# Kernel optimization log

Hardware: AMD Instinct MI355X
Metric: run time of the kernel (lower is better)

## Reference

```python
import jax, jax.numpy as jnp
import numpy as np

B = 65536
OBS_DIM = 85          # input_shape
FEAT = 8              # dim_entity_feature
NL = 5                # dim_landmarks
NT = 10               # dim_total
INF = 64              # in_features == out_features
HID = 64              # rnn_hidden_dim
NACT = 5              # n_actions
ALPHA = 0.01


def _leaky(x):
    return jnp.where(x > 0, x, ALPHA * x)


def setup_inputs() -> dict:
    key = jax.random.key(0)
    ks = jax.random.split(key, 26)
    s = 0.1
    d = {
        'obs': jax.random.normal(ks[0], (B, OBS_DIM), jnp.float32),
        'hidden_state': jax.random.normal(ks[1], (B, HID), jnp.float32),
        # entity input projections (input_layer_0/1/2), stored [in, out]
        'w_in0': jax.random.normal(ks[2], (FEAT, INF), jnp.float32) * s,
        'b_in0': jax.random.normal(ks[3], (INF,), jnp.float32) * s,
        'w_in1': jax.random.normal(ks[4], (FEAT, INF), jnp.float32) * s,
        'b_in1': jax.random.normal(ks[5], (INF,), jnp.float32) * s,
        'w_in2': jax.random.normal(ks[6], (FEAT, INF), jnp.float32) * s,
        'b_in2': jax.random.normal(ks[7], (INF,), jnp.float32) * s,
        # GAT params
        'W': jax.random.normal(ks[8], (INF, INF), jnp.float32) * s,
        'a': jax.random.normal(ks[9], (2 * INF, 1), jnp.float32) * s,
        # output MLP on attention rows (dim_soft = 2*dim_nearby = 10)
        'w_o1': jax.random.normal(ks[10], (2 * NL, 32), jnp.float32) * s,
        'b_o1': jax.random.normal(ks[11], (32,), jnp.float32) * s,
        'w_o2': jax.random.normal(ks[12], (32, 16), jnp.float32) * s,
        'b_o2': jax.random.normal(ks[13], (16,), jnp.float32) * s,
        'w_o3': jax.random.normal(ks[14], (16, 1), jnp.float32) * s,
        'b_o3': jax.random.normal(ks[15], (1,), jnp.float32) * s,
        # fc1 takes obs (85) concat atom_plug (5) -> 90
        'w_fc1': jax.random.normal(ks[16], (OBS_DIM + NL, HID), jnp.float32) * s,
        'b_fc1': jax.random.normal(ks[17], (HID,), jnp.float32) * s,
        # GRUCell, torch layout: [3H, in]
        'w_ih': jax.random.normal(ks[18], (3 * HID, HID), jnp.float32) * s,
        'w_hh': jax.random.normal(ks[19], (3 * HID, HID), jnp.float32) * s,
        'b_ih': jax.random.normal(ks[20], (3 * HID,), jnp.float32) * s,
        'b_hh': jax.random.normal(ks[21], (3 * HID,), jnp.float32) * s,
        'w_fc2': jax.random.normal(ks[22], (HID, NACT), jnp.float32) * s,
        'b_fc2': jax.random.normal(ks[23], (NACT,), jnp.float32) * s,
    }
    return d


def reference(obs, hidden_state, w_in0, b_in0, w_in1, b_in1, w_in2, b_in2,
              W, a, w_o1, b_o1, w_o2, b_o2, w_o3, b_o3,
              w_fc1, b_fc1, w_ih, w_hh, b_ih, b_hh, w_fc2, b_fc2):
    # data_preprocess: drop last dim_nearby cols, rotate first 4 to back, reshape to entities
    o = obs[:, :OBS_DIM - NL]                               # [B, 80]
    obs_in = jnp.concatenate([o[:, 4:], o[:, :4]], axis=-1).reshape(-1, NT, FEAT)  # [B,10,8]

    h0 = _leaky(obs_in @ w_in0 + b_in0)                     # [B,10,64]
    h1 = _leaky(obs_in @ w_in1 + b_in1)
    h2 = _leaky(obs_in @ w_in2 + b_in2)
    h_mix = jnp.concatenate([h0[:, :NL], h1[:, NL:NT - 1], h2[:, NT - 1:NT]], axis=1)  # [B,10,64]

    Wh = h_mix @ W                                          # [B,10,64]
    Wh1 = Wh @ a[:INF]                                      # [B,10,1]
    Wh2 = Wh @ a[INF:]                                      # [B,10,1]
    e = _leaky(Wh1 + jnp.swapaxes(Wh2, 1, 2))               # [B,10,10]

    att0 = jax.nn.softmax(e[:, :NL, NL:], axis=-1)          # [B,5,5]
    att1 = jnp.swapaxes(jax.nn.softmax(e[:, NL:, :NL], axis=-1), 1, 2)  # [B,5,5]
    attention = jnp.concatenate([att0, att1], axis=-1)      # [B,5,10]

    hp = _leaky(attention @ w_o1 + b_o1)
    hp = _leaky(hp @ w_o2 + b_o2)
    hp = _leaky(hp @ w_o3 + b_o3)[..., 0]                   # [B,5]
    obs_out = jax.nn.softmax(hp, axis=-1)                   # [B,5]

    obs_comb = jnp.concatenate([obs, obs_out], axis=-1)     # [B,90]
    x = jax.nn.relu(obs_comb @ w_fc1 + b_fc1)               # [B,64]

    h_in = hidden_state.reshape(-1, HID)
    gi = x @ w_ih.T + b_ih                                  # [B,192]
    gh = h_in @ w_hh.T + b_hh
    r = jax.nn.sigmoid(gi[:, :HID] + gh[:, :HID])
    z = jax.nn.sigmoid(gi[:, HID:2 * HID] + gh[:, HID:2 * HID])
    n = jnp.tanh(gi[:, 2 * HID:] + r * gh[:, 2 * HID:])
    h = (1.0 - z) * n + z * h_in                            # [B,64]

    q = h @ w_fc2 + b_fc2                                   # [B,5]
    return (q, h)
```

## Files before the change

kernel.cpp:

```cpp
#include <hip/hip_runtime.h>
#include <math.h>

namespace {

typedef __bf16 bf16x8 __attribute__((ext_vector_type(8)));
typedef float  f32x4  __attribute__((ext_vector_type(4)));
typedef float  f32x2  __attribute__((ext_vector_type(2)));

constexpr int B_      = 65536;
constexpr int OBS_DIM_= 85;
constexpr int NL_     = 5;
constexpr int NT_     = 10;
constexpr int HID_    = 64;
constexpr int NACT_   = 5;
constexpr float ALPHA_= 0.01f;

__device__ __forceinline__ float leaky(float x)    { return fmaf(fminf(x, 0.0f), ALPHA_ - 1.0f, x); }
__device__ __forceinline__ float sigmoidf(float x) { return 1.0f / (1.0f + __expf(-x)); }
__device__ __forceinline__ float tanh_fast(float x){ return 1.0f - 2.0f / (__expf(2.0f * x) + 1.0f); }

__global__ void prep_kernel(const float* __restrict__ W, const float* __restrict__ a,
                            const float* __restrict__ w_ih, const float* __restrict__ w_hh,
                            const float* __restrict__ w_fc1, void* __restrict__ ws) {
  float* Wa   = (float*)ws;
  __bf16* ih  = (__bf16*)((char*)ws + 512);
  __bf16* hh  = ih + 192 * 64;
  __bf16* f1t = hh + 192 * 64;
  const int tid = blockIdx.x * 256 + threadIdx.x;
  if (blockIdx.x == 0 && threadIdx.x < 64) {
    const int i = threadIdx.x;
    float s1 = 0.0f, s2 = 0.0f;
    #pragma unroll
    for (int j = 0; j < 64; ++j) {
      float w = W[i * 64 + j];
      s1 += w * a[j];
      s2 += w * a[64 + j];
    }
    Wa[i] = s1;
    Wa[64 + i] = s2;
  }
  const int stride = gridDim.x * 256;
  for (int i = tid; i < 192 * 64; i += stride) {
    ih[i] = (__bf16)w_ih[i];
    hh[i] = (__bf16)w_hh[i];
  }
  for (int i = tid; i < 64 * 96; i += stride) {
    int n = i / 96, k = i - 96 * n;
    f1t[i] = (__bf16)(k < 90 ? w_fc1[k * 64 + n] : 0.0f);
  }
}


__global__ __launch_bounds__(256) void front_kernel(
    const float* __restrict__ obs,
    const float* __restrict__ w_in0, const float* __restrict__ b_in0,
    const float* __restrict__ w_in1, const float* __restrict__ b_in1,
    const float* __restrict__ w_in2, const float* __restrict__ b_in2,
    const float* __restrict__ w_o1, const float* __restrict__ b_o1,
    const float* __restrict__ w_o2, const float* __restrict__ b_o2,
    const float* __restrict__ w_o3, const float* __restrict__ b_o3,
    const float* __restrict__ Wa,
    float* __restrict__ out5) {

  __shared__ __align__(16) float s_obs[16][84];
  __shared__ float s_wh1[16][12], s_wh2[16][12];
  __shared__ float s_colm[16][6], s_cols[16][6];
  __shared__ __align__(16) float s_att[16][5][12];
  __shared__ __align__(16) float s_h1[16][5][36];
  __shared__ __align__(16) float s_h2[16][5][20];
  __shared__ float s_hp[16][6];

  const int tid  = threadIdx.x;
  const int wv   = tid >> 6;
  const int lane = tid & 63;
  const int l16  = lane & 15;
  const int rloc = tid >> 4;
  const long gr0 = (long)blockIdx.x * 16;

  {
    const float* src = obs + (gr0 + wv * 4) * OBS_DIM_;
    #pragma unroll
    for (int c0 = 0; c0 < 5; ++c0) {
      int it = c0 * 64 + lane;
      int r = it / 80, c = it - 80 * r;
      s_obs[wv * 4 + r][c] = src[r * OBS_DIM_ + c];
    }
  }

  const int u0 = l16 * 4;
  const float* orow = s_obs[rloc];
  const f32x4 wa1 = *(const f32x4*)&Wa[u0];
  const f32x4 wa2 = *(const f32x4*)&Wa[64 + u0];

  f32x4 wA[8];
  #pragma unroll
  for (int f = 0; f < 8; ++f) wA[f] = *(const f32x4*)&w_in0[f * 64 + u0];
  f32x4 bA = *(const f32x4*)&b_in0[u0];

  #pragma unroll
  for (int t = 0; t < NT_; ++t) {
    if (t == 5) {
      #pragma unroll
      for (int f = 0; f < 8; ++f) wA[f] = *(const f32x4*)&w_in1[f * 64 + u0];
      bA = *(const f32x4*)&b_in1[u0];
    }
    if (t == 9) {
      #pragma unroll
      for (int f = 0; f < 8; ++f) wA[f] = *(const f32x4*)&w_in2[f * 64 + u0];
      bA = *(const f32x4*)&b_in2[u0];
    }
    const int ia = t * 8 + 4;
    int ib = t * 8 + 8;
    if (ib >= 80) ib = 0;
    f32x4 oa = *(const f32x4*)&orow[ia];
    f32x4 ob = *(const f32x4*)&orow[ib];
    f32x4 z = bA;
    #pragma unroll
    for (int f = 0; f < 4; ++f) {
      z[0] += oa[f] * wA[f][0]; z[1] += oa[f] * wA[f][1];
      z[2] += oa[f] * wA[f][2]; z[3] += oa[f] * wA[f][3];
    }
    #pragma unroll
    for (int f = 4; f < 8; ++f) {
      z[0] += ob[f - 4] * wA[f][0]; z[1] += ob[f - 4] * wA[f][1];
      z[2] += ob[f - 4] * wA[f][2]; z[3] += ob[f - 4] * wA[f][3];
    }
    float h0 = leaky(z[0]), h1 = leaky(z[1]), h2 = leaky(z[2]), h3 = leaky(z[3]);
    float p1t = h0 * wa1[0] + h1 * wa1[1] + h2 * wa1[2] + h3 * wa1[3];
    float p2t = h0 * wa2[0] + h1 * wa2[1] + h2 * wa2[2] + h3 * wa2[3];
    p1t += __shfl_xor(p1t, 1, 64);  p2t += __shfl_xor(p2t, 1, 64);
    p1t += __shfl_xor(p1t, 2, 64);  p2t += __shfl_xor(p2t, 2, 64);
    p1t += __shfl_xor(p1t, 4, 64);  p2t += __shfl_xor(p2t, 4, 64);
    p1t += __shfl_xor(p1t, 8, 64);  p2t += __shfl_xor(p2t, 8, 64);
    if (l16 == 0) { s_wh1[rloc][t] = p1t; s_wh2[rloc][t] = p2t; }
  }

  if (l16 >= 5 && l16 < 10) {
    const int jj = l16 - 5;
    float w1v = s_wh1[rloc][NL_ + jj];
    float ev[NL_], m = -1e30f;
    #pragma unroll
    for (int k = 0; k < NL_; ++k) { ev[k] = leaky(w1v + s_wh2[rloc][k]); m = fmaxf(m, ev[k]); }
    float s = 0.0f;
    #pragma unroll
    for (int k = 0; k < NL_; ++k) s += __expf(ev[k] - m);
    s_colm[rloc][jj] = m;
    s_cols[rloc][jj] = s;
  }

  if (l16 < NL_) {
    const int r = l16;
    const float wh1_r = s_wh1[rloc][r];
    const float wh2_r = s_wh2[rloc][r];
    float ev[NL_], m = -1e30f;
    #pragma unroll
    for (int j = 0; j < NL_; ++j) { ev[j] = leaky(wh1_r + s_wh2[rloc][NL_ + j]); m = fmaxf(m, ev[j]); }
    float a0[NL_], s = 0.0f;
    #pragma unroll
    for (int j = 0; j < NL_; ++j) { a0[j] = __expf(ev[j] - m); s += a0[j]; }
    float inv = 1.0f / s;
    #pragma unroll
    for (int j = 0; j < NL_; ++j) s_att[rloc][r][j] = a0[j] * inv;
    #pragma unroll
    for (int jj = 0; jj < NL_; ++jj) {
      float e = leaky(s_wh1[rloc][NL_ + jj] + wh2_r);
      s_att[rloc][r][NL_ + jj] = __expf(e - s_colm[rloc][jj]) / s_cols[rloc][jj];
    }
  }

  {
    f32x2 w1c[NT_];
    #pragma unroll
    for (int k = 0; k < NT_; ++k) w1c[k] = *(const f32x2*)&w_o1[k * 32 + l16 * 2];
    const f32x2 b1 = *(const f32x2*)&b_o1[l16 * 2];
    #pragma unroll
    for (int r5 = 0; r5 < NL_; ++r5) {
      float za = b1[0], zb = b1[1];
      #pragma unroll
      for (int k2 = 0; k2 < 5; ++k2) {
        f32x2 at = *(const f32x2*)&s_att[rloc][r5][k2 * 2];
        za += at[0] * w1c[2 * k2][0] + at[1] * w1c[2 * k2 + 1][0];
        zb += at[0] * w1c[2 * k2][1] + at[1] * w1c[2 * k2 + 1][1];
      }
      *(f32x2*)&s_h1[rloc][r5][l16 * 2] = f32x2{leaky(za), leaky(zb)};
    }
  }

  {
    float w2c[32];
    #pragma unroll
    for (int k = 0; k < 32; ++k) w2c[k] = w_o2[k * 16 + l16];
    const float b2 = b_o2[l16];
    #pragma unroll
    for (int r5 = 0; r5 < NL_; ++r5) {
      float z = b2;
      #pragma unroll
      for (int k4 = 0; k4 < 8; ++k4) {
        f32x4 hv = *(const f32x4*)&s_h1[rloc][r5][k4 * 4];
        z += hv[0] * w2c[4 * k4] + hv[1] * w2c[4 * k4 + 1]
           + hv[2] * w2c[4 * k4 + 2] + hv[3] * w2c[4 * k4 + 3];
      }
      s_h2[rloc][r5][l16] = leaky(z);
    }
  }

  if (l16 < NL_) {
    float z3 = b_o3[0];
    #pragma unroll
    for (int k4 = 0; k4 < 4; ++k4) {
      f32x4 hv = *(const f32x4*)&s_h2[rloc][l16][k4 * 4];
      z3 += hv[0] * w_o3[4 * k4] + hv[1] * w_o3[4 * k4 + 1]
          + hv[2] * w_o3[4 * k4 + 2] + hv[3] * w_o3[4 * k4 + 3];
    }
    float hp_own = leaky(z3);
    s_hp[rloc][l16] = hp_own;
    float m5 = -1e30f;
    #pragma unroll
    for (int j = 0; j < NL_; ++j) m5 = fmaxf(m5, s_hp[rloc][j]);
    float ssum = 0.0f;
    #pragma unroll
    for (int j = 0; j < NL_; ++j) ssum += __expf(s_hp[rloc][j] - m5);
    out5[(gr0 + rloc) * NL_ + l16] = __expf(hp_own - m5) / ssum;
  }
}

constexpr int ROWS_ = 64;
constexpr int SOB_  = 104;
constexpr int SXH_  = 72;

__global__ __launch_bounds__(256) void gemm_kernel(
    const float* __restrict__ obs, const float* __restrict__ hidden,
    const float* __restrict__ b_fc1,
    const float* __restrict__ b_ih, const float* __restrict__ b_hh,
    const float* __restrict__ w_fc2, const float* __restrict__ b_fc2,
    const void* __restrict__ wsv,
    float* q5,
    float* __restrict__ h_out) {

  __shared__ __align__(16) __bf16 A_obs[ROWS_ * SOB_];
  __shared__ __align__(16) __bf16 A_x[ROWS_ * SXH_];

  const int tid  = threadIdx.x;
  const int wv   = tid >> 6;
  const int lane = tid & 63;
  const int l    = lane & 15;
  const int quad = lane >> 4;
  const int r0   = wv * 16;
  const long gr0 = (long)blockIdx.x * ROWS_;

  const __bf16* Wih = (const __bf16*)((const char*)wsv + 512);
  const __bf16* Whh = Wih + 192 * 64;
  const __bf16* Wf1 = Whh + 192 * 64;

  {
    const float* src = obs + (gr0 + r0) * OBS_DIM_;
    #pragma unroll
    for (int k = 0; k < 6; ++k) {
      int idx = lane + 64 * k;
      if (idx < 340) {
        f32x4 v = *(const f32x4*)&src[idx * 4];
        #pragma unroll
        for (int e = 0; e < 4; ++e) {
          int fe = idx * 4 + e;
          int rr = fe / 85, cc = fe - 85 * rr;
          A_obs[(r0 + rr) * SOB_ + cc] = (__bf16)v[e];
        }
      }
    }
    const float* o5 = q5 + (gr0 + r0) * NL_;
    for (int it = lane; it < 16 * NL_; it += 64) {
      int rr = it / NL_; int cc = it - rr * NL_;
      A_obs[(r0 + rr) * SOB_ + 85 + cc] = (__bf16)o5[it];
    }
    for (int it = lane; it < 16 * 6; it += 64) {
      int rr = it / 6; int cc = it - rr * 6;
      A_obs[(r0 + rr) * SOB_ + 90 + cc] = (__bf16)0.0f;
    }
  }

  const f32x4 zero4 = {0.0f, 0.0f, 0.0f, 0.0f};

  bf16x8 ah[2];
  {
    const float* hrow_g = hidden + (gr0 + r0 + l) * HID_;
    #pragma unroll
    for (int ks = 0; ks < 2; ++ks) {
      f32x4 va = *(const f32x4*)&hrow_g[ks * 32 + quad * 8];
      f32x4 vb = *(const f32x4*)&hrow_g[ks * 32 + quad * 8 + 4];
      bf16x8 t;
      t[0] = (__bf16)va[0]; t[1] = (__bf16)va[1]; t[2] = (__bf16)va[2]; t[3] = (__bf16)va[3];
      t[4] = (__bf16)vb[0]; t[5] = (__bf16)vb[1]; t[6] = (__bf16)vb[2]; t[7] = (__bf16)vb[3];
      ah[ks] = t;
    }
  }

  f32x4 cx[4];
  #pragma unroll
  for (int nt = 0; nt < 4; ++nt) cx[nt] = zero4;
  #pragma unroll
  for (int ks = 0; ks < 3; ++ks) {
    bf16x8 af = *(const bf16x8*)&A_obs[(r0 + l) * SOB_ + ks * 32 + quad * 8];
    #pragma unroll
    for (int nt = 0; nt < 4; ++nt) {
      bf16x8 bf = *(const bf16x8*)&Wf1[(nt * 16 + l) * 96 + ks * 32 + quad * 8];
      cx[nt] = __builtin_amdgcn_mfma_f32_16x16x32_bf16(af, bf, cx[nt], 0, 0, 0);
    }
  }
  #pragma unroll
  for (int nt = 0; nt < 4; ++nt) {
    float bias = b_fc1[nt * 16 + l];
    #pragma unroll
    for (int rg = 0; rg < 4; ++rg) {
      float xv = fmaxf(cx[nt][rg] + bias, 0.0f);
      A_x[(r0 + quad * 4 + rg) * SXH_ + nt * 16 + l] = (__bf16)xv;
    }
  }

  bf16x8 ax[2];
  #pragma unroll
  for (int ks = 0; ks < 2; ++ks)
    ax[ks] = *(const bf16x8*)&A_x[(r0 + l) * SXH_ + ks * 32 + quad * 8];

  f32x4 crz[8], cni[4], cnh[4];
  #pragma unroll
  for (int nt = 0; nt < 8; ++nt) crz[nt] = zero4;
  #pragma unroll
  for (int nt = 0; nt < 4; ++nt) { cni[nt] = zero4; cnh[nt] = zero4; }
  #pragma unroll
  for (int nt = 0; nt < 8; ++nt) {
    #pragma unroll
    for (int ks = 0; ks < 2; ++ks) {
      bf16x8 bi = *(const bf16x8*)&Wih[(nt * 16 + l) * 64 + ks * 32 + quad * 8];
      crz[nt] = __builtin_amdgcn_mfma_f32_16x16x32_bf16(ax[ks], bi, crz[nt], 0, 0, 0);
      bf16x8 bh = *(const bf16x8*)&Whh[(nt * 16 + l) * 64 + ks * 32 + quad * 8];
      crz[nt] = __builtin_amdgcn_mfma_f32_16x16x32_bf16(ah[ks], bh, crz[nt], 0, 0, 0);
    }
  }
  #pragma unroll
  for (int nt = 0; nt < 4; ++nt) {
    #pragma unroll
    for (int ks = 0; ks < 2; ++ks) {
      bf16x8 bi = *(const bf16x8*)&Wih[(128 + nt * 16 + l) * 64 + ks * 32 + quad * 8];
      cni[nt] = __builtin_amdgcn_mfma_f32_16x16x32_bf16(ax[ks], bi, cni[nt], 0, 0, 0);
      bf16x8 bh = *(const bf16x8*)&Whh[(128 + nt * 16 + l) * 64 + ks * 32 + quad * 8];
      cnh[nt] = __builtin_amdgcn_mfma_f32_16x16x32_bf16(ah[ks], bh, cnh[nt], 0, 0, 0);
    }
  }

  const long grow = gr0 + r0 + quad * 4;
  float qp[4][NACT_];
  #pragma unroll
  for (int rg = 0; rg < 4; ++rg)
    #pragma unroll
    for (int c = 0; c < NACT_; ++c) qp[rg][c] = 0.0f;

  #pragma unroll
  for (int t = 0; t < 4; ++t) {
    const int ur = t * 16 + l;
    float br  = b_ih[ur] + b_hh[ur];
    float bz  = b_ih[64 + ur] + b_hh[64 + ur];
    float bin = b_ih[128 + ur], bhn = b_hh[128 + ur];
    float w0 = w_fc2[ur * 5 + 0], w1 = w_fc2[ur * 5 + 1], w2 = w_fc2[ur * 5 + 2];
    float w3 = w_fc2[ur * 5 + 3], w4 = w_fc2[ur * 5 + 4];
    #pragma unroll
    for (int rg = 0; rg < 4; ++rg) {
      float rr = sigmoidf(crz[t][rg] + br);
      float zz = sigmoidf(crz[4 + t][rg] + bz);
      float nn = tanh_fast(cni[t][rg] + bin + rr * (cnh[t][rg] + bhn));
      float hold = hidden[(grow + rg) * HID_ + ur];
      float hn = (1.0f - zz) * nn + zz * hold;
      h_out[(grow + rg) * HID_ + ur] = hn;
      qp[rg][0] += hn * w0;
      qp[rg][1] += hn * w1;
      qp[rg][2] += hn * w2;
      qp[rg][3] += hn * w3;
      qp[rg][4] += hn * w4;
    }
  }
  #pragma unroll
  for (int m = 1; m < 16; m <<= 1) {
    #pragma unroll
    for (int rg = 0; rg < 4; ++rg)
      #pragma unroll
      for (int c = 0; c < NACT_; ++c) qp[rg][c] += __shfl_xor(qp[rg][c], m, 64);
  }
  if (l < NACT_) {
    #pragma unroll
    for (int rg = 0; rg < 4; ++rg) {
      float qv = qp[rg][0];
      if (l == 1) qv = qp[rg][1];
      if (l == 2) qv = qp[rg][2];
      if (l == 3) qv = qp[rg][3];
      if (l == 4) qv = qp[rg][4];
      q5[(grow + rg) * NACT_ + l] = qv + b_fc2[l];
    }
  }
}

}

extern "C" void kernel_launch(void* const* d_in, const int* in_sizes, int n_in,
                              void* d_out, int out_size, void* d_ws, size_t ws_size,
                              hipStream_t stream) {
  const float* obs    = (const float*)d_in[0];
  const float* hidden = (const float*)d_in[1];
  const float* w_in0  = (const float*)d_in[2];
  const float* b_in0  = (const float*)d_in[3];
  const float* w_in1  = (const float*)d_in[4];
  const float* b_in1  = (const float*)d_in[5];
  const float* w_in2  = (const float*)d_in[6];
  const float* b_in2  = (const float*)d_in[7];
  const float* W      = (const float*)d_in[8];
  const float* a      = (const float*)d_in[9];
  const float* w_o1   = (const float*)d_in[10];
  const float* b_o1   = (const float*)d_in[11];
  const float* w_o2   = (const float*)d_in[12];
  const float* b_o2   = (const float*)d_in[13];
  const float* w_o3   = (const float*)d_in[14];
  const float* b_o3   = (const float*)d_in[15];
  const float* w_fc1  = (const float*)d_in[16];
  const float* b_fc1  = (const float*)d_in[17];
  const float* w_ih   = (const float*)d_in[18];
  const float* w_hh   = (const float*)d_in[19];
  const float* b_ih   = (const float*)d_in[20];
  const float* b_hh   = (const float*)d_in[21];
  const float* w_fc2  = (const float*)d_in[22];
  const float* b_fc2  = (const float*)d_in[23];

  float* q_out = (float*)d_out;
  float* h_out = q_out + (long)B_ * NACT_;
  const float* Wa = (const float*)d_ws;

  prep_kernel<<<48, 256, 0, stream>>>(W, a, w_ih, w_hh, w_fc1, d_ws);
  front_kernel<<<B_ / 16, 256, 0, stream>>>(
      obs, w_in0, b_in0, w_in1, b_in1, w_in2, b_in2,
      w_o1, b_o1, w_o2, b_o2, w_o3, b_o3, Wa, q_out);
  gemm_kernel<<<B_ / ROWS_, 256, 0, stream>>>(
      obs, hidden, b_fc1, b_ih, b_hh, w_fc2, b_fc2, d_ws, q_out, h_out);
}
```

Measured before the change: 206.4 us.

## Permute GRU weight rows for vectorized epilogue and batch global loads early

```diff
diff --git a/kernel.cpp b/kernel.cpp
--- a/kernel.cpp
+++ b/kernel.cpp
@@ -41,15 +41,18 @@
   }
   const int stride = gridDim.x * 256;
   for (int i = tid; i < 192 * 64; i += stride) {
-    ih[i] = (__bf16)w_ih[i];
-    hh[i] = (__bf16)w_hh[i];
+    int pr = i >> 6, k = i & 63;
+    int g  = pr >> 6;
+    int q  = pr & 63;
+    int orig = (g << 6) + ((q & 15) << 2) + (q >> 4);
+    ih[i] = (__bf16)w_ih[orig * 64 + k];
+    hh[i] = (__bf16)w_hh[orig * 64 + k];
   }
   for (int i = tid; i < 64 * 96; i += stride) {
     int n = i / 96, k = i - 96 * n;
     f1t[i] = (__bf16)(k < 90 ? w_fc1[k * 64 + n] : 0.0f);
   }
 }
-
 
 __global__ __launch_bounds__(256) void front_kernel(
     const float* __restrict__ obs,
@@ -228,7 +231,7 @@
 constexpr int SOB_  = 104;
 constexpr int SXH_  = 72;
 
-__global__ __launch_bounds__(256) void gemm_kernel(
+__global__ __launch_bounds__(256, 4) void gemm_kernel(
     const float* __restrict__ obs, const float* __restrict__ hidden,
     const float* __restrict__ b_fc1,
     const float* __restrict__ b_ih, const float* __restrict__ b_hh,
@@ -252,47 +255,72 @@
   const __bf16* Whh = Wih + 192 * 64;
   const __bf16* Wf1 = Whh + 192 * 64;
 
-  {
-    const float* src = obs + (gr0 + r0) * OBS_DIM_;
-    #pragma unroll
-    for (int k = 0; k < 6; ++k) {
-      int idx = lane + 64 * k;
-      if (idx < 340) {
-        f32x4 v = *(const f32x4*)&src[idx * 4];
-        #pragma unroll
-        for (int e = 0; e < 4; ++e) {
-          int fe = idx * 4 + e;
-          int rr = fe / 85, cc = fe - 85 * rr;
-          A_obs[(r0 + rr) * SOB_ + cc] = (__bf16)v[e];
-        }
+  const float* src = obs + (gr0 + r0) * OBS_DIM_;
+  f32x4 vobs[6];
+  #pragma unroll
+  for (int k = 0; k < 6; ++k) {
+    int idx = lane + 64 * k;
+    if (idx < 340) vobs[k] = *(const f32x4*)&src[idx * 4];
+  }
+  const float* o5 = q5 + (gr0 + r0) * NL_;
+  float vo5a = o5[lane];
+  float vo5b = (lane < 16) ? o5[lane + 64] : 0.0f;
+
+  const float* hrow_g = hidden + (gr0 + r0 + l) * HID_;
+  f32x4 vha0 = *(const f32x4*)&hrow_g[quad * 8];
+  f32x4 vha1 = *(const f32x4*)&hrow_g[quad * 8 + 4];
+  f32x4 vhb0 = *(const f32x4*)&hrow_g[32 + quad * 8];
+  f32x4 vhb1 = *(const f32x4*)&hrow_g[32 + quad * 8 + 4];
+
+  bf16x8 bf1[3][4];
+  #pragma unroll
+  for (int ks = 0; ks < 3; ++ks)
+    #pragma unroll
+    for (int nt = 0; nt < 4; ++nt)
+      bf1[ks][nt] = *(const bf16x8*)&Wf1[(nt * 16 + l) * 96 + ks * 32 + quad * 8];
+
+  #pragma unroll
+  for (int k = 0; k < 6; ++k) {
+    int idx = lane + 64 * k;
+    if (idx < 340) {
+      #pragma unroll
+      for (int e = 0; e < 4; ++e) {
+        int fe = idx * 4 + e;
+        int rr = fe / 85, cc = fe - 85 * rr;
+        A_obs[(r0 + rr) * SOB_ + cc] = (__bf16)vobs[k][e];
       }
     }
-    const float* o5 = q5 + (gr0 + r0) * NL_;
-    for (int it = lane; it < 16 * NL_; it += 64) {
-      int rr = it / NL_; int cc = it - rr * NL_;
-      A_obs[(r0 + rr) * SOB_ + 85 + cc] = (__bf16)o5[it];
-    }
-    for (int it = lane; it < 16 * 6; it += 64) {
-      int rr = it / 6; int cc = it - rr * 6;
+  }
+  {
+    int rr = lane / NL_, cc = lane - NL_ * rr;
+    A_obs[(r0 + rr) * SOB_ + 85 + cc] = (__bf16)vo5a;
+  }
+  if (lane < 16) {
+    int it = lane + 64;
+    int rr = it / NL_, cc = it - NL_ * rr;
+    A_obs[(r0 + rr) * SOB_ + 85 + cc] = (__bf16)vo5b;
+  }
+  #pragma unroll
+  for (int p = 0; p < 2; ++p) {
+    int it = lane + 64 * p;
+    if (it < 96) {
+      int rr = it / 6, cc = it - 6 * rr;
       A_obs[(r0 + rr) * SOB_ + 90 + cc] = (__bf16)0.0f;
     }
   }
 
+  bf16x8 ah[2];
+  {
+    bf16x8 t;
+    t[0] = (__bf16)vha0[0]; t[1] = (__bf16)vha0[1]; t[2] = (__bf16)vha0[2]; t[3] = (__bf16)vha0[3];
+    t[4] = (__bf16)vha1[0]; t[5] = (__bf16)vha1[1]; t[6] = (__bf16)vha1[2]; t[7] = (__bf16)vha1[3];
+    ah[0] = t;
+    t[0] = (__bf16)vhb0[0]; t[1] = (__bf16)vhb0[1]; t[2] = (__bf16)vhb0[2]; t[3] = (__bf16)vhb0[3];
+    t[4] = (__bf16)vhb1[0]; t[5] = (__bf16)vhb1[1]; t[6] = (__bf16)vhb1[2]; t[7] = (__bf16)vhb1[3];
+    ah[1] = t;
+  }
+
   const f32x4 zero4 = {0.0f, 0.0f, 0.0f, 0.0f};
-
-  bf16x8 ah[2];
-  {
-    const float* hrow_g = hidden + (gr0 + r0 + l) * HID_;
-    #pragma unroll
-    for (int ks = 0; ks < 2; ++ks) {
-      f32x4 va = *(const f32x4*)&hrow_g[ks * 32 + quad * 8];
-      f32x4 vb = *(const f32x4*)&hrow_g[ks * 32 + quad * 8 + 4];
-      bf16x8 t;
-      t[0] = (__bf16)va[0]; t[1] = (__bf16)va[1]; t[2] = (__bf16)va[2]; t[3] = (__bf16)va[3];
-      t[4] = (__bf16)vb[0]; t[5] = (__bf16)vb[1]; t[6] = (__bf16)vb[2]; t[7] = (__bf16)vb[3];
-      ah[ks] = t;
-    }
-  }
 
   f32x4 cx[4];
   #pragma unroll
@@ -301,10 +329,8 @@
   for (int ks = 0; ks < 3; ++ks) {
     bf16x8 af = *(const bf16x8*)&A_obs[(r0 + l) * SOB_ + ks * 32 + quad * 8];
     #pragma unroll
-    for (int nt = 0; nt < 4; ++nt) {
-      bf16x8 bf = *(const bf16x8*)&Wf1[(nt * 16 + l) * 96 + ks * 32 + quad * 8];
-      cx[nt] = __builtin_amdgcn_mfma_f32_16x16x32_bf16(af, bf, cx[nt], 0, 0, 0);
-    }
+    for (int nt = 0; nt < 4; ++nt)
+      cx[nt] = __builtin_amdgcn_mfma_f32_16x16x32_bf16(af, bf1[ks][nt], cx[nt], 0, 0, 0);
   }
   #pragma unroll
   for (int nt = 0; nt < 4; ++nt) {
@@ -348,6 +374,22 @@
   }
 
   const long grow = gr0 + r0 + quad * 4;
+
+  f32x4 br4, bz4, bin4, bhn4;
+  {
+    f32x4 a0 = *(const f32x4*)&b_ih[4 * l];
+    f32x4 a1 = *(const f32x4*)&b_hh[4 * l];
+    br4 = a0 + a1;
+    a0 = *(const f32x4*)&b_ih[64 + 4 * l];
+    a1 = *(const f32x4*)&b_hh[64 + 4 * l];
+    bz4 = a0 + a1;
+    bin4 = *(const f32x4*)&b_ih[128 + 4 * l];
+    bhn4 = *(const f32x4*)&b_hh[128 + 4 * l];
+  }
+  f32x4 w20[5];
+  #pragma unroll
+  for (int j = 0; j < 5; ++j) w20[j] = *(const f32x4*)&w_fc2[20 * l + 4 * j];
+
   float qp[4][NACT_];
   #pragma unroll
   for (int rg = 0; rg < 4; ++rg)
@@ -355,28 +397,23 @@
     for (int c = 0; c < NACT_; ++c) qp[rg][c] = 0.0f;
 
   #pragma unroll
-  for (int t = 0; t < 4; ++t) {
-    const int ur = t * 16 + l;
-    float br  = b_ih[ur] + b_hh[ur];
-    float bz  = b_ih[64 + ur] + b_hh[64 + ur];
-    float bin = b_ih[128 + ur], bhn = b_hh[128 + ur];
-    float w0 = w_fc2[ur * 5 + 0], w1 = w_fc2[ur * 5 + 1], w2 = w_fc2[ur * 5 + 2];
-    float w3 = w_fc2[ur * 5 + 3], w4 = w_fc2[ur * 5 + 4];
-    #pragma unroll
-    for (int rg = 0; rg < 4; ++rg) {
-      float rr = sigmoidf(crz[t][rg] + br);
-      float zz = sigmoidf(crz[4 + t][rg] + bz);
-      float nn = tanh_fast(cni[t][rg] + bin + rr * (cnh[t][rg] + bhn));
-      float hold = hidden[(grow + rg) * HID_ + ur];
-      float hn = (1.0f - zz) * nn + zz * hold;
-      h_out[(grow + rg) * HID_ + ur] = hn;
-      qp[rg][0] += hn * w0;
-      qp[rg][1] += hn * w1;
-      qp[rg][2] += hn * w2;
-      qp[rg][3] += hn * w3;
-      qp[rg][4] += hn * w4;
-    }
-  }
+  for (int rg = 0; rg < 4; ++rg) {
+    f32x4 hold = *(const f32x4*)&hidden[(grow + rg) * HID_ + 4 * l];
+    f32x4 hnew;
+    #pragma unroll
+    for (int t = 0; t < 4; ++t) {
+      float rr = sigmoidf(crz[t][rg] + br4[t]);
+      float zz = sigmoidf(crz[4 + t][rg] + bz4[t]);
+      float nn = tanh_fast(cni[t][rg] + bin4[t] + rr * (cnh[t][rg] + bhn4[t]));
+      float hn = (1.0f - zz) * nn + zz * hold[t];
+      hnew[t] = hn;
+      #pragma unroll
+      for (int c = 0; c < NACT_; ++c)
+        qp[rg][c] += hn * w20[(5 * t + c) >> 2][(5 * t + c) & 3];
+    }
+    *(f32x4*)&h_out[(grow + rg) * HID_ + 4 * l] = hnew;
+  }
+
   #pragma unroll
   for (int m = 1; m < 16; m <<= 1) {
     #pragma unroll
```

New measurement: 202.5 us. No clear change (-1.9%).
